# Kernel tuning notes

Hardware: AMD Instinct MI355X
Metric: run time of the kernel (lower is better)

## Reference

```python
import jax, jax.numpy as jnp
import numpy as np

HEADS = 8
EPS = 1e-6


def _conv1x1(w, t):
    # w: [out_c, in_c], t: [B, in_c, L] -> [B, out_c, L]
    return jnp.einsum('oc,bcl->bol', w, t)


def setup_inputs() -> dict:
    key = jax.random.key(0)
    ks = jax.random.split(key, 9)
    B, C, H, W = 8, 256, 128, 128
    dim = C
    s = 1.0 / np.sqrt(dim)
    x = jax.random.normal(ks[0], (B, C, H, W), dtype=jnp.float32)
    y = jax.random.normal(ks[1], (B, 1, H // 2, W // 2), dtype=jnp.float32)
    wq_x = jax.random.normal(ks[2], (dim, dim), dtype=jnp.float32) * s
    wk_x = jax.random.normal(ks[3], (dim, dim), dtype=jnp.float32) * s
    wv = jax.random.normal(ks[4], (dim, dim), dtype=jnp.float32) * s
    wq_y = jax.random.normal(ks[5], (dim, 1), dtype=jnp.float32)
    wk_y = jax.random.normal(ks[6], (dim, 1), dtype=jnp.float32)
    w_out = jax.random.normal(ks[7], (dim, dim), dtype=jnp.float32) * s
    b_out = jnp.zeros((dim,), dtype=jnp.float32)
    return {"x": x, "y": y, "wq_x": wq_x, "wk_x": wk_x, "wv": wv,
            "wq_y": wq_y, "wk_y": wk_y, "w_out": w_out, "b_out": b_out}


def reference(x, y, wq_x, wk_x, wv, wq_y, wk_y, w_out, b_out):
    B, C, H, W = x.shape
    h = HEADS
    d = C // h
    L = H * W
    xr = x.reshape(B, C, L)

    # bilinear upsample y to (H, W); jax.image 'bilinear' == torch align_corners=False
    y_up = jax.image.resize(y, (B, 1, H, W), method='bilinear')
    yr = y_up.reshape(B, 1, L)

    q_x = _conv1x1(wq_x, xr).reshape(B, h, d, L)
    k_x = _conv1x1(wk_x, xr).reshape(B, h, d, L)
    v = _conv1x1(wv, xr).reshape(B, h, d, L)
    q_y = _conv1x1(wq_y, yr).reshape(B, h, d, L)
    k_y = _conv1x1(wk_y, yr).reshape(B, h, d, L)

    q = jax.nn.elu(q_x * q_y) + 1.0
    k = jax.nn.elu(k_x * k_y) + 1.0

    kv = jnp.einsum('bhcl,bhdl->bhcd', k, v)      # [B,h,d,d]
    k_sum = k.sum(axis=-1)                        # [B,h,d]
    z = 1.0 / (jnp.einsum('bhcl,bhc->bhl', q, k_sum) + EPS)  # [B,h,L]
    # faithful to torch: out[b,h,c,l] = q[b,h,c,l] * sum_d kv[b,h,c,d] * z[b,h,l]
    out = jnp.einsum('bhcl,bhcd,bhl->bhcl', q, kv, z)

    out = out.reshape(B, C, L)
    out = _conv1x1(w_out, out) + b_out[None, :, None]
    return out.reshape(B, C, H, W)
```

## Files before the change

### kernel.cpp

```cpp
#include <hip/hip_runtime.h>
#include <hip/hip_bf16.h>

typedef unsigned short u16;
typedef unsigned int   u32;
using short8   = __attribute__((ext_vector_type(8))) short;
using f32x4    = __attribute__((ext_vector_type(4))) float;
using ushort4v = __attribute__((ext_vector_type(4))) unsigned short;
using u32x4    = __attribute__((ext_vector_type(4))) unsigned int;

#define CDIM 256
#define LDIM 16384
#define LT   128
#define NT   128
#define NB   8

__device__ __forceinline__ u16 f2bf(float f) {
  u32 u = __float_as_uint(f);
  u = (u + 0x7FFFu + ((u >> 16) & 1u)) >> 16;
  return (u16)u;
}

__device__ __forceinline__ u32 pk2(float a, float b) {
  __hip_bfloat162 h = __float22bfloat162_rn(make_float2(a, b));
  return *(u32*)&h;
}

__device__ __forceinline__ int swz(int l) {
  return ((l >> 2) & 31) ^ ((l & 3) << 2);
}

__device__ __forceinline__ short8 frag_b(const char* xl, int ll, int kk, int g) {
  int slot = (kk * 4 + g) ^ swz(ll);
  return *(const short8*)(xl + (size_t)ll * 512 + slot * 16);
}

__global__ void k_prep(const float* __restrict__ wq_x, const float* __restrict__ wk_x,
                       const float* __restrict__ w_out, const float* __restrict__ wv,
                       const float* __restrict__ y,
                       u16* __restrict__ wqx_bf, u16* __restrict__ wkx_bf,
                       u16* __restrict__ wout_bf, u16* __restrict__ wvsum_bf,
                       float* __restrict__ yup) {
  int id = blockIdx.x * 256 + threadIdx.x;
  if (id < 65536) {
    wqx_bf[id]  = f2bf(wq_x[id]);
    wkx_bf[id]  = f2bf(wk_x[id]);
    wout_bf[id] = f2bf(w_out[id]);
  }
  if (id < 4096) {
    int r = id >> 8, c = id & 255;
    float s = 0.f;
    if (r < 8) {
      for (int d2 = 0; d2 < 32; ++d2) s += wv[(r * 32 + d2) * 256 + c];
    }
    wvsum_bf[id] = f2bf(s);
  }
  if (id < 131072) {
    int b = id >> 14, rem = id & 16383, i = rem >> 7, j = rem & 127;
    float si = 0.5f * i - 0.25f, sj = 0.5f * j - 0.25f;
    int i0 = (int)floorf(si), j0 = (int)floorf(sj);
    float fi = si - (float)i0, fj = sj - (float)j0;
    int i0c = i0 < 0 ? 0 : i0, i1c = i0 + 1 > 63 ? 63 : i0 + 1;
    int j0c = j0 < 0 ? 0 : j0, j1c = j0 + 1 > 63 ? 63 : j0 + 1;
    const float* yb = y + b * 4096;
    float v = (1.f - fi) * ((1.f - fj) * yb[i0c * 64 + j0c] + fj * yb[i0c * 64 + j1c])
            +        fi  * ((1.f - fj) * yb[i1c * 64 + j0c] + fj * yb[i1c * 64 + j1c]);
    yup[id] = v;
  }
}

__device__ __forceinline__ void stage_x(char* xl, const float* __restrict__ x,
                                        int b, int l0, int tid) {
  int k = tid & 31, co = tid >> 5;
  const float* bp = x + ((size_t)b * 256 + co * 8) * LDIM + l0 + k * 4;
#pragma unroll
  for (int oi = 0; oi < 4; ++oi) {
    const float* p = bp + (size_t)(oi * 64) * LDIM;
    float4 r0 = *(const float4*)(p + 0 * LDIM);
    float4 r1 = *(const float4*)(p + 1 * LDIM);
    float4 r2 = *(const float4*)(p + 2 * LDIM);
    float4 r3 = *(const float4*)(p + 3 * LDIM);
    float4 r4 = *(const float4*)(p + 4 * LDIM);
    float4 r5 = *(const float4*)(p + 5 * LDIM);
    float4 r6 = *(const float4*)(p + 6 * LDIM);
    float4 r7 = *(const float4*)(p + 7 * LDIM);
    const float* f0 = (const float*)&r0; const float* f1 = (const float*)&r1;
    const float* f2 = (const float*)&r2; const float* f3 = (const float*)&r3;
    const float* f4 = (const float*)&r4; const float* f5 = (const float*)&r5;
    const float* f6 = (const float*)&r6; const float* f7 = (const float*)&r7;
    int so = co + oi * 8;
#pragma unroll
    for (int e = 0; e < 4; ++e) {
      int l = k * 4 + e;
      u32x4 wv;
      wv.x = pk2(f0[e], f1[e]);
      wv.y = pk2(f2[e], f3[e]);
      wv.z = pk2(f4[e], f5[e]);
      wv.w = pk2(f6[e], f7[e]);
      int slot = so ^ swz(l);
      *(u32x4*)(xl + (size_t)l * 512 + slot * 16) = wv;
    }
  }
}

__global__ __launch_bounds__(256, 2) void k_pass1(
    const float* __restrict__ x, const u16* __restrict__ wkx_bf,
    const u16* __restrict__ wvsum_bf, const float* __restrict__ wk_y,
    const float* __restrict__ yup, float* __restrict__ part) {
  __shared__ u32x4 xbuf[4096];
  __shared__ float vsum_lds[8 * 128];
  __shared__ float yup_lds[128];
  __shared__ float wky_lds[256];
  char* xl = (char*)xbuf;

  int tid = threadIdx.x, bid = blockIdx.x;
  int b = bid >> 7, tile = bid & 127;
  int l0 = tile * LT;

  if (tid < 128) yup_lds[tid] = yup[b * LDIM + l0 + tid];
  wky_lds[tid] = wk_y[tid];
  stage_x(xl, x, b, l0, tid);
  __syncthreads();

  int lane = tid & 63, wave = tid >> 6;
  int lid = lane & 15, g = lane >> 4;
  int wb = wave * 64;

  f32x4 z4 = {0.f, 0.f, 0.f, 0.f};
  f32x4 acc[4][8];
#pragma unroll
  for (int i = 0; i < 4; ++i)
#pragma unroll
    for (int j = 0; j < 8; ++j) acc[i][j] = z4;
  f32x4 vacc[2] = {z4, z4};

  for (int kk = 0; kk < 8; ++kk) {
    int kof = kk * 32 + g * 8;
    short8 a[4];
#pragma unroll
    for (int fm = 0; fm < 4; ++fm)
      a[fm] = *(const short8*)(wkx_bf + (size_t)(wb + fm * 16 + lid) * 256 + kof);
    short8 av = *(const short8*)(wvsum_bf + (size_t)lid * 256 + kof);
#pragma unroll
    for (int fn = 0; fn < 8; ++fn) {
      short8 bb = frag_b(xl, fn * 16 + lid, kk, g);
#pragma unroll
      for (int fm = 0; fm < 4; ++fm)
        acc[fm][fn] = __builtin_amdgcn_mfma_f32_16x16x32_bf16(a[fm], bb, acc[fm][fn], 0, 0, 0);
    }
#pragma unroll
    for (int fv = 0; fv < 2; ++fv) {
      short8 bb = frag_b(xl, (wave * 2 + fv) * 16 + lid, kk, g);
      vacc[fv] = __builtin_amdgcn_mfma_f32_16x16x32_bf16(av, bb, vacc[fv], 0, 0, 0);
    }
  }
  if (g < 2) {
#pragma unroll
    for (int fv = 0; fv < 2; ++fv)
#pragma unroll
      for (int r = 0; r < 4; ++r)
        vsum_lds[(g * 4 + r) * 128 + (wave * 2 + fv) * 16 + lid] = vacc[fv][r];
  }
  __syncthreads();

  float wky_r[4][4];
#pragma unroll
  for (int fm = 0; fm < 4; ++fm)
#pragma unroll
    for (int r = 0; r < 4; ++r) wky_r[fm][r] = wky_lds[wb + fm * 16 + g * 4 + r];

  float s1[4][4], s2[4][4];
#pragma unroll
  for (int fm = 0; fm < 4; ++fm)
#pragma unroll
    for (int r = 0; r < 4; ++r) { s1[fm][r] = 0.f; s2[fm][r] = 0.f; }

#pragma unroll
  for (int fn = 0; fn < 8; ++fn) {
    int l = fn * 16 + lid;
    float yv = yup_lds[l];
#pragma unroll
    for (int fm = 0; fm < 4; ++fm) {
      float vs = vsum_lds[(wave * 2 + (fm >> 1)) * 128 + l];
#pragma unroll
      for (int r = 0; r < 4; ++r) {
        float v = acc[fm][fn][r] * (wky_r[fm][r] * yv);
        float kq = v > 0.f ? v + 1.f : __expf(v);
        s1[fm][r] += kq;
        s2[fm][r] += kq * vs;
      }
    }
  }
#pragma unroll
  for (int fm = 0; fm < 4; ++fm)
#pragma unroll
    for (int r = 0; r < 4; ++r) {
      float a1 = s1[fm][r], a2 = s2[fm][r];
#pragma unroll
      for (int off = 1; off < 16; off <<= 1) {
        a1 += __shfl_xor(a1, off);
        a2 += __shfl_xor(a2, off);
      }
      if (lid == 0) {
        int c = wb + fm * 16 + g * 4 + r;
        part[(size_t)bid * 512 + c]       = a1;
        part[(size_t)bid * 512 + 256 + c] = a2;
      }
    }
}

__global__ __launch_bounds__(1024) void k_reduce(
    const float* __restrict__ part, float* __restrict__ ksum, float* __restrict__ kvs) {
  __shared__ float red[2][512];
  int b = blockIdx.x, tid = threadIdx.x;
  int u = tid & 511, h = tid >> 9;
  float s = 0.f;
  for (int j = 0; j < 64; ++j)
    s += part[(size_t)(b * NT + h * 64 + j) * 512 + u];
  red[h][u] = s;
  __syncthreads();
  if (tid < 512) {
    float t = red[0][tid] + red[1][tid];
    if (tid < 256) ksum[b * 256 + tid] = t;
    else           kvs[b * 256 + tid - 256] = t;
  }
}

__global__ __launch_bounds__(256, 2) void k_pass2(
    const float* __restrict__ x, const u16* __restrict__ wqx_bf,
    const u16* __restrict__ wout_bf, const float* __restrict__ wq_y,
    const float* __restrict__ yup, const float* __restrict__ ksum,
    const float* __restrict__ kvs, const float* __restrict__ b_out,
    float* __restrict__ out) {
  __shared__ u32x4 xbuf[4096];
  __shared__ float yup_lds[128];
  __shared__ float wqy_lds[256];
  __shared__ float ksum_lds[256];
  __shared__ float kvs_lds[256];
  __shared__ float bout_lds[256];
  char* xl = (char*)xbuf;

  int tid = threadIdx.x, bid = blockIdx.x;
  int b = bid >> 7, tile = bid & 127;
  int l0 = tile * LT;

  if (tid < 128) yup_lds[tid] = yup[b * LDIM + l0 + tid];
  wqy_lds[tid]  = wq_y[tid];
  ksum_lds[tid] = ksum[b * 256 + tid];
  kvs_lds[tid]  = kvs[b * 256 + tid];
  bout_lds[tid] = b_out[tid];
  stage_x(xl, x, b, l0, tid);
  __syncthreads();

  int lane = tid & 63, wave = tid >> 6;
  int lid = lane & 15, g = lane >> 4;
  int wb = wave * 64;

  f32x4 z4 = {0.f, 0.f, 0.f, 0.f};
  f32x4 acc[4][8];
#pragma unroll
  for (int i = 0; i < 4; ++i)
#pragma unroll
    for (int j = 0; j < 8; ++j) acc[i][j] = z4;

  for (int kk = 0; kk < 8; ++kk) {
    int kof = kk * 32 + g * 8;
    short8 a[4];
#pragma unroll
    for (int fm = 0; fm < 4; ++fm)
      a[fm] = *(const short8*)(wqx_bf + (size_t)(wb + fm * 16 + lid) * 256 + kof);
#pragma unroll
    for (int fn = 0; fn < 8; ++fn) {
      short8 bb = frag_b(xl, fn * 16 + lid, kk, g);
#pragma unroll
      for (int fm = 0; fm < 4; ++fm)
        acc[fm][fn] = __builtin_amdgcn_mfma_f32_16x16x32_bf16(a[fm], bb, acc[fm][fn], 0, 0, 0);
    }
  }
  __syncthreads();

  float wqy_r[4][4], ks_r[4][4], kv_r[4][4];
#pragma unroll
  for (int fm = 0; fm < 4; ++fm)
#pragma unroll
    for (int r = 0; r < 4; ++r) {
      int c = wb + fm * 16 + g * 4 + r;
      wqy_r[fm][r] = wqy_lds[c];
      ks_r[fm][r]  = ksum_lds[c];
      kv_r[fm][r]  = kvs_lds[c];
    }

#pragma unroll
  for (int fn = 0; fn < 8; ++fn) {
    int l = fn * 16 + lid;
    float yv = yup_lds[l];
    float q[4][4];
    float d0 = 0.f, d1 = 0.f;
#pragma unroll
    for (int fm = 0; fm < 4; ++fm)
#pragma unroll
      for (int r = 0; r < 4; ++r) {
        float v = acc[fm][fn][r] * (wqy_r[fm][r] * yv);
        float qq = v > 0.f ? v + 1.f : __expf(v);
        q[fm][r] = qq;
        if (fm < 2) d0 += qq * ks_r[fm][r]; else d1 += qq * ks_r[fm][r];
      }
    d0 += __shfl_xor(d0, 16); d0 += __shfl_xor(d0, 32);
    d1 += __shfl_xor(d1, 16); d1 += __shfl_xor(d1, 32);
    float zz0 = 1.f / (d0 + 1e-6f), zz1 = 1.f / (d1 + 1e-6f);
#pragma unroll
    for (int fm = 0; fm < 4; ++fm) {
      float zz = fm < 2 ? zz0 : zz1;
      ushort4v tw;
#pragma unroll
      for (int r = 0; r < 4; ++r) tw[r] = f2bf(q[fm][r] * kv_r[fm][r] * zz);
      int slot = (wave * 8 + fm * 2 + (g >> 1)) ^ swz(l);
      *(ushort4v*)(xl + (size_t)l * 512 + slot * 16 + (g & 1) * 8) = tw;
    }
  }
  __syncthreads();

#pragma unroll
  for (int i = 0; i < 4; ++i)
#pragma unroll
    for (int j = 0; j < 8; ++j) acc[i][j] = z4;
  for (int kk = 0; kk < 8; ++kk) {
    int kof = kk * 32 + g * 8;
    short8 a[4];
#pragma unroll
    for (int fm = 0; fm < 4; ++fm)
      a[fm] = *(const short8*)(wout_bf + (size_t)(wb + fm * 16 + lid) * 256 + kof);
#pragma unroll
    for (int fn = 0; fn < 8; ++fn) {
      short8 bb = frag_b(xl, fn * 16 + lid, kk, g);
#pragma unroll
      for (int fm = 0; fm < 4; ++fm)
        acc[fm][fn] = __builtin_amdgcn_mfma_f32_16x16x32_bf16(a[fm], bb, acc[fm][fn], 0, 0, 0);
    }
  }

#pragma unroll
  for (int fm = 0; fm < 4; ++fm) {
#pragma unroll
    for (int r = 0; r < 4; ++r) {
      int o = wb + fm * 16 + g * 4 + r;
      float bo = bout_lds[o];
      size_t base = ((size_t)b * 256 + o) * LDIM + l0;
#pragma unroll
      for (int fn = 0; fn < 8; ++fn)
        out[base + fn * 16 + lid] = acc[fm][fn][r] + bo;
    }
  }
}

extern "C" void kernel_launch(void* const* d_in, const int* in_sizes, int n_in,
                              void* d_out, int out_size, void* d_ws, size_t ws_size,
                              hipStream_t stream) {
  const float* x     = (const float*)d_in[0];
  const float* y     = (const float*)d_in[1];
  const float* wq_x  = (const float*)d_in[2];
  const float* wk_x  = (const float*)d_in[3];
  const float* wv    = (const float*)d_in[4];
  const float* wq_y  = (const float*)d_in[5];
  const float* wk_y  = (const float*)d_in[6];
  const float* w_out = (const float*)d_in[7];
  const float* b_out = (const float*)d_in[8];
  float* out = (float*)d_out;

  char* ws = (char*)d_ws;
  float* yup      = (float*)(ws + 0);
  u16*   wqx_bf   = (u16*)(ws + 524288);
  u16*   wkx_bf   = (u16*)(ws + 655360);
  u16*   wout_bf  = (u16*)(ws + 786432);
  u16*   wvsum_bf = (u16*)(ws + 917504);
  float* ksum     = (float*)(ws + 925696);
  float* kvs      = (float*)(ws + 933888);
  float* part     = (float*)(ws + 942080);

  k_prep<<<512, 256, 0, stream>>>(wq_x, wk_x, w_out, wv, y,
                                  wqx_bf, wkx_bf, wout_bf, wvsum_bf, yup);
  k_pass1<<<NB * NT, 256, 0, stream>>>(x, wkx_bf, wvsum_bf, wk_y, yup, part);
  k_reduce<<<NB, 1024, 0, stream>>>(part, ksum, kvs);
  k_pass2<<<NB * NT, 256, 0, stream>>>(x, wqx_bf, wout_bf, wq_y, yup,
                                       ksum, kvs, b_out, out);
}
```

Before: 153.0 us.

## Compute Q in pass1, store bf16 Q image, fold kv into per-batch w_out

Measured after the change: 192.2 us. 25.6% more time.

```diff
diff --git a/kernel.cpp b/kernel.cpp
--- a/kernel.cpp
+++ b/kernel.cpp
@@ -8,10 +8,9 @@
 using ushort4v = __attribute__((ext_vector_type(4))) unsigned short;
 using u32x4    = __attribute__((ext_vector_type(4))) unsigned int;
 
-#define CDIM 256
 #define LDIM 16384
-#define LT   128
-#define NT   128
+#define LT   64
+#define NT   256
 #define NB   8
 
 __device__ __forceinline__ u16 f2bf(float f) {
@@ -19,7 +18,9 @@
   u = (u + 0x7FFFu + ((u >> 16) & 1u)) >> 16;
   return (u16)u;
 }
-
+__device__ __forceinline__ float bf2f(u16 h) {
+  return __uint_as_float((u32)h << 16);
+}
 __device__ __forceinline__ u32 pk2(float a, float b) {
   __hip_bfloat162 h = __float22bfloat162_rn(make_float2(a, b));
   return *(u32*)&h;
@@ -28,23 +29,19 @@
 __device__ __forceinline__ int swz(int l) {
   return ((l >> 2) & 31) ^ ((l & 3) << 2);
 }
-
 __device__ __forceinline__ short8 frag_b(const char* xl, int ll, int kk, int g) {
   int slot = (kk * 4 + g) ^ swz(ll);
   return *(const short8*)(xl + (size_t)ll * 512 + slot * 16);
 }
 
 __global__ void k_prep(const float* __restrict__ wq_x, const float* __restrict__ wk_x,
-                       const float* __restrict__ w_out, const float* __restrict__ wv,
-                       const float* __restrict__ y,
+                       const float* __restrict__ wv, const float* __restrict__ y,
                        u16* __restrict__ wqx_bf, u16* __restrict__ wkx_bf,
-                       u16* __restrict__ wout_bf, u16* __restrict__ wvsum_bf,
-                       float* __restrict__ yup) {
+                       u16* __restrict__ wvsum_bf, float* __restrict__ yup) {
   int id = blockIdx.x * 256 + threadIdx.x;
   if (id < 65536) {
-    wqx_bf[id]  = f2bf(wq_x[id]);
-    wkx_bf[id]  = f2bf(wk_x[id]);
-    wout_bf[id] = f2bf(w_out[id]);
+    wqx_bf[id] = f2bf(wq_x[id]);
+    wkx_bf[id] = f2bf(wk_x[id]);
   }
   if (id < 4096) {
     int r = id >> 8, c = id & 255;
@@ -68,56 +65,61 @@
   }
 }
 
+__device__ __forceinline__ void stage_one_octet(char* xl, const float* p, int so, int k) {
+  float4 r0 = *(const float4*)(p + 0 * LDIM);
+  float4 r1 = *(const float4*)(p + 1 * LDIM);
+  float4 r2 = *(const float4*)(p + 2 * LDIM);
+  float4 r3 = *(const float4*)(p + 3 * LDIM);
+  float4 r4 = *(const float4*)(p + 4 * LDIM);
+  float4 r5 = *(const float4*)(p + 5 * LDIM);
+  float4 r6 = *(const float4*)(p + 6 * LDIM);
+  float4 r7 = *(const float4*)(p + 7 * LDIM);
+  const float* f0 = (const float*)&r0; const float* f1 = (const float*)&r1;
+  const float* f2 = (const float*)&r2; const float* f3 = (const float*)&r3;
+  const float* f4 = (const float*)&r4; const float* f5 = (const float*)&r5;
+  const float* f6 = (const float*)&r6; const float* f7 = (const float*)&r7;
+#pragma unroll
+  for (int e = 0; e < 4; ++e) {
+    int l = k * 4 + e;
+    u32x4 wv;
+    wv.x = pk2(f0[e], f1[e]);
+    wv.y = pk2(f2[e], f3[e]);
+    wv.z = pk2(f4[e], f5[e]);
+    wv.w = pk2(f6[e], f7[e]);
+    int slot = so ^ swz(l);
+    *(u32x4*)(xl + (size_t)l * 512 + slot * 16) = wv;
+  }
+}
+
 __device__ __forceinline__ void stage_x(char* xl, const float* __restrict__ x,
                                         int b, int l0, int tid) {
-  int k = tid & 31, co = tid >> 5;
-  const float* bp = x + ((size_t)b * 256 + co * 8) * LDIM + l0 + k * 4;
-#pragma unroll
-  for (int oi = 0; oi < 4; ++oi) {
-    const float* p = bp + (size_t)(oi * 64) * LDIM;
-    float4 r0 = *(const float4*)(p + 0 * LDIM);
-    float4 r1 = *(const float4*)(p + 1 * LDIM);
-    float4 r2 = *(const float4*)(p + 2 * LDIM);
-    float4 r3 = *(const float4*)(p + 3 * LDIM);
-    float4 r4 = *(const float4*)(p + 4 * LDIM);
-    float4 r5 = *(const float4*)(p + 5 * LDIM);
-    float4 r6 = *(const float4*)(p + 6 * LDIM);
-    float4 r7 = *(const float4*)(p + 7 * LDIM);
-    const float* f0 = (const float*)&r0; const float* f1 = (const float*)&r1;
-    const float* f2 = (const float*)&r2; const float* f3 = (const float*)&r3;
-    const float* f4 = (const float*)&r4; const float* f5 = (const float*)&r5;
-    const float* f6 = (const float*)&r6; const float* f7 = (const float*)&r7;
-    int so = co + oi * 8;
-#pragma unroll
-    for (int e = 0; e < 4; ++e) {
-      int l = k * 4 + e;
-      u32x4 wv;
-      wv.x = pk2(f0[e], f1[e]);
-      wv.y = pk2(f2[e], f3[e]);
-      wv.z = pk2(f4[e], f5[e]);
-      wv.w = pk2(f6[e], f7[e]);
-      int slot = so ^ swz(l);
-      *(u32x4*)(xl + (size_t)l * 512 + slot * 16) = wv;
-    }
-  }
+  int k = tid & 15, cog = tid >> 4;
+  const float* bp = x + ((size_t)b * 256 + cog * 8) * LDIM + l0 + k * 4;
+#pragma unroll 1
+  for (int oi = 0; oi < 2; ++oi)
+    stage_one_octet(xl, bp + (size_t)(oi * 128) * LDIM, cog + oi * 16, k);
 }
 
 __global__ __launch_bounds__(256, 2) void k_pass1(
     const float* __restrict__ x, const u16* __restrict__ wkx_bf,
-    const u16* __restrict__ wvsum_bf, const float* __restrict__ wk_y,
-    const float* __restrict__ yup, float* __restrict__ part) {
-  __shared__ u32x4 xbuf[4096];
-  __shared__ float vsum_lds[8 * 128];
-  __shared__ float yup_lds[128];
+    const u16* __restrict__ wqx_bf, const u16* __restrict__ wvsum_bf,
+    const float* __restrict__ wk_y, const float* __restrict__ wq_y,
+    const float* __restrict__ yup, u16* __restrict__ qimg,
+    float* __restrict__ part) {
+  __shared__ u32x4 xbuf[2048];
+  __shared__ float vsum_lds[8 * 64];
+  __shared__ float yup_lds[64];
   __shared__ float wky_lds[256];
+  __shared__ float wqy_lds[256];
   char* xl = (char*)xbuf;
 
   int tid = threadIdx.x, bid = blockIdx.x;
-  int b = bid >> 7, tile = bid & 127;
+  int b = bid >> 8, tile = bid & 255;
   int l0 = tile * LT;
 
-  if (tid < 128) yup_lds[tid] = yup[b * LDIM + l0 + tid];
+  if (tid < 64) yup_lds[tid] = yup[b * LDIM + l0 + tid];
   wky_lds[tid] = wk_y[tid];
+  wqy_lds[tid] = wq_y[tid];
   stage_x(xl, x, b, l0, tid);
   __syncthreads();
 
@@ -126,39 +128,38 @@
   int wb = wave * 64;
 
   f32x4 z4 = {0.f, 0.f, 0.f, 0.f};
-  f32x4 acc[4][8];
+  f32x4 acck[4][4], accq[4][4];
 #pragma unroll
   for (int i = 0; i < 4; ++i)
 #pragma unroll
-    for (int j = 0; j < 8; ++j) acc[i][j] = z4;
-  f32x4 vacc[2] = {z4, z4};
+    for (int j = 0; j < 4; ++j) { acck[i][j] = z4; accq[i][j] = z4; }
+  f32x4 vacc = z4;
 
   for (int kk = 0; kk < 8; ++kk) {
     int kof = kk * 32 + g * 8;
-    short8 a[4];
-#pragma unroll
-    for (int fm = 0; fm < 4; ++fm)
-      a[fm] = *(const short8*)(wkx_bf + (size_t)(wb + fm * 16 + lid) * 256 + kof);
+    short8 ak[4], aq[4];
+#pragma unroll
+    for (int fm = 0; fm < 4; ++fm) {
+      ak[fm] = *(const short8*)(wkx_bf + (size_t)(wb + fm * 16 + lid) * 256 + kof);
+      aq[fm] = *(const short8*)(wqx_bf + (size_t)(wb + fm * 16 + lid) * 256 + kof);
+    }
     short8 av = *(const short8*)(wvsum_bf + (size_t)lid * 256 + kof);
 #pragma unroll
-    for (int fn = 0; fn < 8; ++fn) {
+    for (int fn = 0; fn < 4; ++fn) {
       short8 bb = frag_b(xl, fn * 16 + lid, kk, g);
 #pragma unroll
-      for (int fm = 0; fm < 4; ++fm)
-        acc[fm][fn] = __builtin_amdgcn_mfma_f32_16x16x32_bf16(a[fm], bb, acc[fm][fn], 0, 0, 0);
-    }
-#pragma unroll
-    for (int fv = 0; fv < 2; ++fv) {
-      short8 bb = frag_b(xl, (wave * 2 + fv) * 16 + lid, kk, g);
-      vacc[fv] = __builtin_amdgcn_mfma_f32_16x16x32_bf16(av, bb, vacc[fv], 0, 0, 0);
-    }
+      for (int fm = 0; fm < 4; ++fm) {
+        acck[fm][fn] = __builtin_amdgcn_mfma_f32_16x16x32_bf16(ak[fm], bb, acck[fm][fn], 0, 0, 0);
+        accq[fm][fn] = __builtin_amdgcn_mfma_f32_16x16x32_bf16(aq[fm], bb, accq[fm][fn], 0, 0, 0);
+      }
+    }
+    short8 bv = frag_b(xl, wave * 16 + lid, kk, g);
+    vacc = __builtin_amdgcn_mfma_f32_16x16x32_bf16(av, bv, vacc, 0, 0, 0);
   }
   if (g < 2) {
 #pragma unroll
-    for (int fv = 0; fv < 2; ++fv)
-#pragma unroll
-      for (int r = 0; r < 4; ++r)
-        vsum_lds[(g * 4 + r) * 128 + (wave * 2 + fv) * 16 + lid] = vacc[fv][r];
+    for (int r = 0; r < 4; ++r)
+      vsum_lds[(g * 4 + r) * 64 + wave * 16 + lid] = vacc[r];
   }
   __syncthreads();
 
@@ -175,15 +176,15 @@
     for (int r = 0; r < 4; ++r) { s1[fm][r] = 0.f; s2[fm][r] = 0.f; }
 
 #pragma unroll
-  for (int fn = 0; fn < 8; ++fn) {
+  for (int fn = 0; fn < 4; ++fn) {
     int l = fn * 16 + lid;
     float yv = yup_lds[l];
 #pragma unroll
     for (int fm = 0; fm < 4; ++fm) {
-      float vs = vsum_lds[(wave * 2 + (fm >> 1)) * 128 + l];
+      float vs = vsum_lds[(wave * 2 + (fm >> 1)) * 64 + l];
 #pragma unroll
       for (int r = 0; r < 4; ++r) {
-        float v = acc[fm][fn][r] * (wky_r[fm][r] * yv);
+        float v = acck[fm][fn][r] * (wky_r[fm][r] * yv);
         float kq = v > 0.f ? v + 1.f : __expf(v);
         s1[fm][r] += kq;
         s2[fm][r] += kq * vs;
@@ -206,131 +207,153 @@
         part[(size_t)bid * 512 + 256 + c] = a2;
       }
     }
-}
-
-__global__ __launch_bounds__(1024) void k_reduce(
-    const float* __restrict__ part, float* __restrict__ ksum, float* __restrict__ kvs) {
+
+  float wqy_r[4][4];
+#pragma unroll
+  for (int fm = 0; fm < 4; ++fm)
+#pragma unroll
+    for (int r = 0; r < 4; ++r) wqy_r[fm][r] = wqy_lds[wb + fm * 16 + g * 4 + r];
+
+#pragma unroll
+  for (int fn = 0; fn < 4; ++fn) {
+    int l = fn * 16 + lid;
+    float yv = yup_lds[l];
+#pragma unroll
+    for (int fm = 0; fm < 4; ++fm) {
+      ushort4v tw;
+#pragma unroll
+      for (int r = 0; r < 4; ++r) {
+        float v = accq[fm][fn][r] * (wqy_r[fm][r] * yv);
+        float qq = v > 0.f ? v + 1.f : __expf(v);
+        tw[r] = f2bf(qq);
+      }
+      int slot = (wave * 8 + fm * 2 + (g >> 1)) ^ swz(l);
+      *(ushort4v*)(xl + (size_t)l * 512 + slot * 16 + (g & 1) * 8) = tw;
+    }
+  }
+  __syncthreads();
+
+  char* qdst = (char*)(qimg) + (size_t)bid * 32768;
+#pragma unroll
+  for (int i = 0; i < 8; ++i)
+    *(u32x4*)(qdst + i * 4096 + tid * 16) = *(const u32x4*)(xl + i * 4096 + tid * 16);
+}
+
+__global__ __launch_bounds__(1024) void k_mid(
+    const float* __restrict__ part, const float* __restrict__ w_out,
+    u16* __restrict__ ksrows, u16* __restrict__ woutp) {
   __shared__ float red[2][512];
+  __shared__ float ks_lds[256];
+  __shared__ float kv_lds[256];
   int b = blockIdx.x, tid = threadIdx.x;
   int u = tid & 511, h = tid >> 9;
   float s = 0.f;
-  for (int j = 0; j < 64; ++j)
-    s += part[(size_t)(b * NT + h * 64 + j) * 512 + u];
+  for (int j = 0; j < 128; ++j)
+    s += part[(size_t)(b * NT + h * 128 + j) * 512 + u];
   red[h][u] = s;
   __syncthreads();
   if (tid < 512) {
     float t = red[0][tid] + red[1][tid];
-    if (tid < 256) ksum[b * 256 + tid] = t;
-    else           kvs[b * 256 + tid - 256] = t;
-  }
-}
-
-__global__ __launch_bounds__(256, 2) void k_pass2(
-    const float* __restrict__ x, const u16* __restrict__ wqx_bf,
-    const u16* __restrict__ wout_bf, const float* __restrict__ wq_y,
-    const float* __restrict__ yup, const float* __restrict__ ksum,
-    const float* __restrict__ kvs, const float* __restrict__ b_out,
+    if (tid < 256) ks_lds[tid] = t;
+    else           kv_lds[tid - 256] = t;
+  }
+  __syncthreads();
+  u16* kr = ksrows + b * 4096;
+  for (int j = tid; j < 4096; j += 1024) {
+    int r = j >> 8, c = j & 255;
+    int hh = c >> 5;
+    float ks = ks_lds[c];
+    u16 hi = f2bf(ks);
+    u16 val = 0;
+    if (r == 2 * hh) val = hi;
+    else if (r == 2 * hh + 1) val = f2bf(ks - bf2f(hi));
+    kr[j] = val;
+  }
+  u16* wp = woutp + (size_t)b * 65536;
+  for (int j = tid; j < 65536; j += 1024)
+    wp[j] = f2bf(w_out[j] * kv_lds[j & 255]);
+}
+
+__global__ __launch_bounds__(256, 3) void k_pass2(
+    const u16* __restrict__ qimg, const u16* __restrict__ woutp,
+    const u16* __restrict__ ksrows, const float* __restrict__ b_out,
     float* __restrict__ out) {
-  __shared__ u32x4 xbuf[4096];
-  __shared__ float yup_lds[128];
-  __shared__ float wqy_lds[256];
-  __shared__ float ksum_lds[256];
-  __shared__ float kvs_lds[256];
+  __shared__ u32x4 xbuf[2048];
+  __shared__ float zden_lds[8 * 64];
   __shared__ float bout_lds[256];
   char* xl = (char*)xbuf;
 
   int tid = threadIdx.x, bid = blockIdx.x;
-  int b = bid >> 7, tile = bid & 127;
+  int b = bid >> 8, tile = bid & 255;
   int l0 = tile * LT;
-
-  if (tid < 128) yup_lds[tid] = yup[b * LDIM + l0 + tid];
-  wqy_lds[tid]  = wq_y[tid];
-  ksum_lds[tid] = ksum[b * 256 + tid];
-  kvs_lds[tid]  = kvs[b * 256 + tid];
-  bout_lds[tid] = b_out[tid];
-  stage_x(xl, x, b, l0, tid);
-  __syncthreads();
-
   int lane = tid & 63, wave = tid >> 6;
   int lid = lane & 15, g = lane >> 4;
+
+  bout_lds[tid] = b_out[tid];
+  const char* gsrc = (const char*)qimg + (size_t)bid * 32768;
+#pragma unroll
+  for (int it = 0; it < 8; ++it) {
+    int idx = it * 4 + wave;
+    __builtin_amdgcn_global_load_lds(
+        (const __attribute__((address_space(1))) void*)(gsrc + idx * 1024 + lane * 16),
+        (__attribute__((address_space(3))) void*)(xl + idx * 1024),
+        16, 0, 0);
+  }
+  __syncthreads();
+
+  f32x4 z4 = {0.f, 0.f, 0.f, 0.f};
+  f32x4 zacc = z4;
+  const u16* krb = ksrows + b * 4096;
+  for (int kk = 0; kk < 8; ++kk) {
+    int kof = kk * 32 + g * 8;
+    short8 av = *(const short8*)(krb + lid * 256 + kof);
+    short8 bv = frag_b(xl, wave * 16 + lid, kk, g);
+    zacc = __builtin_amdgcn_mfma_f32_16x16x32_bf16(av, bv, zacc, 0, 0, 0);
+  }
+  {
+    int l = wave * 16 + lid;
+    zden_lds[(2 * g) * 64 + l]     = zacc[0] + zacc[1];
+    zden_lds[(2 * g + 1) * 64 + l] = zacc[2] + zacc[3];
+  }
+  __syncthreads();
+
+  {
+    int l = tid & 63, grp = tid >> 6;
+#pragma unroll
+    for (int jo = 0; jo < 8; ++jo) {
+      int o = grp * 8 + jo;
+      int slot = o ^ swz(l);
+      char* p = xl + (size_t)l * 512 + slot * 16;
+      u32x4 v = *(u32x4*)p;
+      float zz = 1.f / (zden_lds[(o >> 2) * 64 + l] + 1e-6f);
+      u32x4 w;
+#pragma unroll
+      for (int q4 = 0; q4 < 4; ++q4) {
+        u32 val = v[q4];
+        float lo = bf2f((u16)(val & 0xffff)) * zz;
+        float hi = bf2f((u16)(val >> 16)) * zz;
+        w[q4] = pk2(lo, hi);
+      }
+      *(u32x4*)p = w;
+    }
+  }
+  __syncthreads();
+
+  f32x4 acc[4][4];
+#pragma unroll
+  for (int i = 0; i < 4; ++i)
+#pragma unroll
+    for (int j = 0; j < 4; ++j) acc[i][j] = z4;
   int wb = wave * 64;
-
-  f32x4 z4 = {0.f, 0.f, 0.f, 0.f};
-  f32x4 acc[4][8];
-#pragma unroll
-  for (int i = 0; i < 4; ++i)
-#pragma unroll
-    for (int j = 0; j < 8; ++j) acc[i][j] = z4;
-
+  const u16* wpb = woutp + (size_t)b * 65536;
   for (int kk = 0; kk < 8; ++kk) {
     int kof = kk * 32 + g * 8;
     short8 a[4];
 #pragma unroll
     for (int fm = 0; fm < 4; ++fm)
-      a[fm] = *(const short8*)(wqx_bf + (size_t)(wb + fm * 16 + lid) * 256 + kof);
-#pragma unroll
-    for (int fn = 0; fn < 8; ++fn) {
-      short8 bb = frag_b(xl, fn * 16 + lid, kk, g);
-#pragma unroll
-      for (int fm = 0; fm < 4; ++fm)
-        acc[fm][fn] = __builtin_amdgcn_mfma_f32_16x16x32_bf16(a[fm], bb, acc[fm][fn], 0, 0, 0);
-    }
-  }
-  __syncthreads();
-
-  float wqy_r[4][4], ks_r[4][4], kv_r[4][4];
-#pragma unroll
-  for (int fm = 0; fm < 4; ++fm)
-#pragma unroll
-    for (int r = 0; r < 4; ++r) {
-      int c = wb + fm * 16 + g * 4 + r;
-      wqy_r[fm][r] = wqy_lds[c];
-      ks_r[fm][r]  = ksum_lds[c];
-      kv_r[fm][r]  = kvs_lds[c];
-    }
-
-#pragma unroll
-  for (int fn = 0; fn < 8; ++fn) {
-    int l = fn * 16 + lid;
-    float yv = yup_lds[l];
-    float q[4][4];
-    float d0 = 0.f, d1 = 0.f;
-#pragma unroll
-    for (int fm = 0; fm < 4; ++fm)
-#pragma unroll
-      for (int r = 0; r < 4; ++r) {
-        float v = acc[fm][fn][r] * (wqy_r[fm][r] * yv);
-        float qq = v > 0.f ? v + 1.f : __expf(v);
-        q[fm][r] = qq;
-        if (fm < 2) d0 += qq * ks_r[fm][r]; else d1 += qq * ks_r[fm][r];
-      }
-    d0 += __shfl_xor(d0, 16); d0 += __shfl_xor(d0, 32);
-    d1 += __shfl_xor(d1, 16); d1 += __shfl_xor(d1, 32);
-    float zz0 = 1.f / (d0 + 1e-6f), zz1 = 1.f / (d1 + 1e-6f);
-#pragma unroll
-    for (int fm = 0; fm < 4; ++fm) {
-      float zz = fm < 2 ? zz0 : zz1;
-      ushort4v tw;
-#pragma unroll
-      for (int r = 0; r < 4; ++r) tw[r] = f2bf(q[fm][r] * kv_r[fm][r] * zz);
-      int slot = (wave * 8 + fm * 2 + (g >> 1)) ^ swz(l);
-      *(ushort4v*)(xl + (size_t)l * 512 + slot * 16 + (g & 1) * 8) = tw;
-    }
-  }
-  __syncthreads();
-
-#pragma unroll
-  for (int i = 0; i < 4; ++i)
-#pragma unroll
-    for (int j = 0; j < 8; ++j) acc[i][j] = z4;
-  for (int kk = 0; kk < 8; ++kk) {
-    int kof = kk * 32 + g * 8;
-    short8 a[4];
-#pragma unroll
-    for (int fm = 0; fm < 4; ++fm)
-      a[fm] = *(const short8*)(wout_bf + (size_t)(wb + fm * 16 + lid) * 256 + kof);
-#pragma unroll
-    for (int fn = 0; fn < 8; ++fn) {
+      a[fm] = *(const short8*)(wpb + (size_t)(wb + fm * 16 + lid) * 256 + kof);
+#pragma unroll
+    for (int fn = 0; fn < 4; ++fn) {
       short8 bb = frag_b(xl, fn * 16 + lid, kk, g);
 #pragma unroll
       for (int fm = 0; fm < 4; ++fm)
@@ -346,7 +369,7 @@
       float bo = bout_lds[o];
       size_t base = ((size_t)b * 256 + o) * LDIM + l0;
 #pragma unroll
-      for (int fn = 0; fn < 8; ++fn)
+      for (int fn = 0; fn < 4; ++fn)
         out[base + fn * 16 + lid] = acc[fm][fn][r] + bo;
     }
   }
@@ -367,19 +390,18 @@
   float* out = (float*)d_out;
 
   char* ws = (char*)d_ws;
-  float* yup      = (float*)(ws + 0);
-  u16*   wqx_bf   = (u16*)(ws + 524288);
-  u16*   wkx_bf   = (u16*)(ws + 655360);
-  u16*   wout_bf  = (u16*)(ws + 786432);
-  u16*   wvsum_bf = (u16*)(ws + 917504);
-  float* ksum     = (float*)(ws + 925696);
-  float* kvs      = (float*)(ws + 933888);
-  float* part     = (float*)(ws + 942080);
-
-  k_prep<<<512, 256, 0, stream>>>(wq_x, wk_x, w_out, wv, y,
-                                  wqx_bf, wkx_bf, wout_bf, wvsum_bf, yup);
-  k_pass1<<<NB * NT, 256, 0, stream>>>(x, wkx_bf, wvsum_bf, wk_y, yup, part);
-  k_reduce<<<NB, 1024, 0, stream>>>(part, ksum, kvs);
-  k_pass2<<<NB * NT, 256, 0, stream>>>(x, wqx_bf, wout_bf, wq_y, yup,
-                                       ksum, kvs, b_out, out);
-}
+  u16*   qimg     = (u16*)(ws + 0);
+  float* part     = (float*)(ws + 67108864);
+  float* yup      = (float*)(ws + 71303168);
+  u16*   wqx_bf   = (u16*)(ws + 71827456);
+  u16*   wkx_bf   = (u16*)(ws + 71958528);
+  u16*   wvsum_bf = (u16*)(ws + 72089600);
+  u16*   ksrows   = (u16*)(ws + 72097792);
+  u16*   woutp    = (u16*)(ws + 72163328);
+
+  k_prep<<<512, 256, 0, stream>>>(wq_x, wk_x, wv, y, wqx_bf, wkx_bf, wvsum_bf, yup);
+  k_pass1<<<NB * NT, 256, 0, stream>>>(x, wkx_bf, wqx_bf, wvsum_bf, wk_y, wq_y,
+                                       yup, qimg, part);
+  k_mid<<<NB, 1024, 0, stream>>>(part, w_out, ksrows, woutp);
+  k_pass2<<<NB * NT, 256, 0, stream>>>(qimg, woutp, ksrows, b_out, out);
+}
```

## Precompute bf16 swizzled x tiles once and stream them into LDS directly

Applied to the files above, without the earlier changes.

After: 184.5 us. 1.21x slower.

```diff
diff --git a/kernel.cpp b/kernel.cpp
--- a/kernel.cpp
+++ b/kernel.cpp
@@ -8,7 +8,6 @@
 using ushort4v = __attribute__((ext_vector_type(4))) unsigned short;
 using u32x4    = __attribute__((ext_vector_type(4))) unsigned int;
 
-#define CDIM 256
 #define LDIM 16384
 #define LT   128
 #define NT   128
@@ -28,7 +27,6 @@
 __device__ __forceinline__ int swz(int l) {
   return ((l >> 2) & 31) ^ ((l & 3) << 2);
 }
-
 __device__ __forceinline__ short8 frag_b(const char* xl, int ll, int kk, int g) {
   int slot = (kk * 4 + g) ^ swz(ll);
   return *(const short8*)(xl + (size_t)ll * 512 + slot * 16);
@@ -68,42 +66,59 @@
   }
 }
 
-__device__ __forceinline__ void stage_x(char* xl, const float* __restrict__ x,
-                                        int b, int l0, int tid) {
+__device__ __forceinline__ void conv_one_octet(char* dst, const float* p, int so, int k) {
+  float4 r0 = *(const float4*)(p + 0 * LDIM);
+  float4 r1 = *(const float4*)(p + 1 * LDIM);
+  float4 r2 = *(const float4*)(p + 2 * LDIM);
+  float4 r3 = *(const float4*)(p + 3 * LDIM);
+  float4 r4 = *(const float4*)(p + 4 * LDIM);
+  float4 r5 = *(const float4*)(p + 5 * LDIM);
+  float4 r6 = *(const float4*)(p + 6 * LDIM);
+  float4 r7 = *(const float4*)(p + 7 * LDIM);
+  const float* f0 = (const float*)&r0; const float* f1 = (const float*)&r1;
+  const float* f2 = (const float*)&r2; const float* f3 = (const float*)&r3;
+  const float* f4 = (const float*)&r4; const float* f5 = (const float*)&r5;
+  const float* f6 = (const float*)&r6; const float* f7 = (const float*)&r7;
+#pragma unroll
+  for (int e = 0; e < 4; ++e) {
+    int l = k * 4 + e;
+    u32x4 wv;
+    wv.x = pk2(f0[e], f1[e]);
+    wv.y = pk2(f2[e], f3[e]);
+    wv.z = pk2(f4[e], f5[e]);
+    wv.w = pk2(f6[e], f7[e]);
+    int slot = so ^ swz(l);
+    *(u32x4*)(dst + (size_t)l * 512 + slot * 16) = wv;
+  }
+}
+
+__global__ __launch_bounds__(256) void k_conv(const float* __restrict__ x,
+                                              u16* __restrict__ xbf) {
+  int tid = threadIdx.x, bid = blockIdx.x;
+  int b = bid >> 7, tile = bid & 127;
+  int l0 = tile * LT;
   int k = tid & 31, co = tid >> 5;
+  char* dst = (char*)xbf + (size_t)bid * 65536;
   const float* bp = x + ((size_t)b * 256 + co * 8) * LDIM + l0 + k * 4;
-#pragma unroll
-  for (int oi = 0; oi < 4; ++oi) {
-    const float* p = bp + (size_t)(oi * 64) * LDIM;
-    float4 r0 = *(const float4*)(p + 0 * LDIM);
-    float4 r1 = *(const float4*)(p + 1 * LDIM);
-    float4 r2 = *(const float4*)(p + 2 * LDIM);
-    float4 r3 = *(const float4*)(p + 3 * LDIM);
-    float4 r4 = *(const float4*)(p + 4 * LDIM);
-    float4 r5 = *(const float4*)(p + 5 * LDIM);
-    float4 r6 = *(const float4*)(p + 6 * LDIM);
-    float4 r7 = *(const float4*)(p + 7 * LDIM);
-    const float* f0 = (const float*)&r0; const float* f1 = (const float*)&r1;
-    const float* f2 = (const float*)&r2; const float* f3 = (const float*)&r3;
-    const float* f4 = (const float*)&r4; const float* f5 = (const float*)&r5;
-    const float* f6 = (const float*)&r6; const float* f7 = (const float*)&r7;
-    int so = co + oi * 8;
-#pragma unroll
-    for (int e = 0; e < 4; ++e) {
-      int l = k * 4 + e;
-      u32x4 wv;
-      wv.x = pk2(f0[e], f1[e]);
-      wv.y = pk2(f2[e], f3[e]);
-      wv.z = pk2(f4[e], f5[e]);
-      wv.w = pk2(f6[e], f7[e]);
-      int slot = so ^ swz(l);
-      *(u32x4*)(xl + (size_t)l * 512 + slot * 16) = wv;
-    }
+#pragma unroll 1
+  for (int oi = 0; oi < 4; ++oi)
+    conv_one_octet(dst, bp + (size_t)(oi * 64) * LDIM, co + oi * 8, k);
+}
+
+__device__ __forceinline__ void gload_tile(char* xl, const char* gsrc, int tid) {
+  int lane = tid & 63, wave = tid >> 6;
+#pragma unroll
+  for (int it = 0; it < 16; ++it) {
+    int idx = it * 4 + wave;
+    __builtin_amdgcn_global_load_lds(
+        (const __attribute__((address_space(1))) void*)(gsrc + idx * 1024 + lane * 16),
+        (__attribute__((address_space(3))) void*)(xl + idx * 1024),
+        16, 0, 0);
   }
 }
 
 __global__ __launch_bounds__(256, 2) void k_pass1(
-    const float* __restrict__ x, const u16* __restrict__ wkx_bf,
+    const u16* __restrict__ xbf, const u16* __restrict__ wkx_bf,
     const u16* __restrict__ wvsum_bf, const float* __restrict__ wk_y,
     const float* __restrict__ yup, float* __restrict__ part) {
   __shared__ u32x4 xbuf[4096];
@@ -118,7 +133,7 @@
 
   if (tid < 128) yup_lds[tid] = yup[b * LDIM + l0 + tid];
   wky_lds[tid] = wk_y[tid];
-  stage_x(xl, x, b, l0, tid);
+  gload_tile(xl, (const char*)xbf + (size_t)bid * 65536, tid);
   __syncthreads();
 
   int lane = tid & 63, wave = tid >> 6;
@@ -226,7 +241,7 @@
 }
 
 __global__ __launch_bounds__(256, 2) void k_pass2(
-    const float* __restrict__ x, const u16* __restrict__ wqx_bf,
+    const u16* __restrict__ xbf, const u16* __restrict__ wqx_bf,
     const u16* __restrict__ wout_bf, const float* __restrict__ wq_y,
     const float* __restrict__ yup, const float* __restrict__ ksum,
     const float* __restrict__ kvs, const float* __restrict__ b_out,
@@ -248,7 +263,7 @@
   ksum_lds[tid] = ksum[b * 256 + tid];
   kvs_lds[tid]  = kvs[b * 256 + tid];
   bout_lds[tid] = b_out[tid];
-  stage_x(xl, x, b, l0, tid);
+  gload_tile(xl, (const char*)xbf + (size_t)bid * 65536, tid);
   __syncthreads();
 
   int lane = tid & 63, wave = tid >> 6;
@@ -375,11 +390,13 @@
   float* ksum     = (float*)(ws + 925696);
   float* kvs      = (float*)(ws + 933888);
   float* part     = (float*)(ws + 942080);
+  u16*   xbf      = (u16*)(ws + 4194304);
 
   k_prep<<<512, 256, 0, stream>>>(wq_x, wk_x, w_out, wv, y,
                                   wqx_bf, wkx_bf, wout_bf, wvsum_bf, yup);
-  k_pass1<<<NB * NT, 256, 0, stream>>>(x, wkx_bf, wvsum_bf, wk_y, yup, part);
+  k_conv<<<NB * NT, 256, 0, stream>>>(x, xbf);
+  k_pass1<<<NB * NT, 256, 0, stream>>>(xbf, wkx_bf, wvsum_bf, wk_y, yup, part);
   k_reduce<<<NB, 1024, 0, stream>>>(part, ksum, kvs);
-  k_pass2<<<NB * NT, 256, 0, stream>>>(x, wqx_bf, wout_bf, wq_y, yup,
+  k_pass2<<<NB * NT, 256, 0, stream>>>(xbf, wqx_bf, wout_bf, wq_y, yup,
                                        ksum, kvs, b_out, out);
 }
```
